# Kernel optimization log

Hardware: AMD Instinct MI355X
Metric: run time of the kernel (lower is better)

The kernel has to match this reference:

```python
import jax, jax.numpy as jnp
import numpy as np

N = 100000   # nodes
E = 1600000  # edges (avg degree 16)
IN, H, OUT, P = 100, 256, 256, 128
EPS = 1e-5


def setup_inputs() -> dict:
    key = jax.random.key(0)
    ks = jax.random.split(key, 12)

    def lin(k, o, i):
        return jax.random.normal(k, (o, i), jnp.float32) / np.float32(np.sqrt(i))

    return {
        "x": jax.random.normal(ks[0], (N, IN), jnp.float32),
        "edge_index": jax.random.randint(ks[1], (2, E), 0, N),
        # SAGEConv l (aggregated-neighbor branch, has bias) and r (root branch, no bias)
        "Wl0": lin(ks[2], H, IN), "bl0": jnp.zeros((H,), jnp.float32), "Wr0": lin(ks[3], H, IN),
        "Wl1": lin(ks[4], H, H),  "bl1": jnp.zeros((H,), jnp.float32), "Wr1": lin(ks[5], H, H),
        "Wl2": lin(ks[6], OUT, H), "bl2": jnp.zeros((OUT,), jnp.float32), "Wr2": lin(ks[7], OUT, H),
        # projection head + BatchNorm1d(128)
        "Wp": lin(ks[8], P, OUT), "bp": jnp.zeros((P,), jnp.float32),
        "gamma": jnp.ones((P,), jnp.float32), "beta": jnp.zeros((P,), jnp.float32),
    }


def _sage_conv(x, src, dst, Wl, bl, Wr):
    # PyG SAGEConv default: mean-aggregate source features into destinations,
    # then lin_l(agg) + lin_r(x).
    agg = jax.ops.segment_sum(x[src], dst, num_segments=N)           # [N, d]
    deg = jax.ops.segment_sum(jnp.ones((src.shape[0],), x.dtype), dst, num_segments=N)
    agg = agg / jnp.maximum(deg, 1.0)[:, None]
    return agg @ Wl.T + bl + x @ Wr.T


def reference(x, edge_index, Wl0, bl0, Wr0, Wl1, bl1, Wr1, Wl2, bl2, Wr2, Wp, bp, gamma, beta):
    src, dst = edge_index[0], edge_index[1]
    x = jax.nn.relu(_sage_conv(x, src, dst, Wl0, bl0, Wr0))  # dropout is identity in eval
    x = jax.nn.relu(_sage_conv(x, src, dst, Wl1, bl1, Wr1))
    x = _sage_conv(x, src, dst, Wl2, bl2, Wr2)               # no relu on last layer
    z = x @ Wp.T + bp                                        # projection head -> [N, 128]
    mu = jnp.mean(z, axis=0)
    var = jnp.var(z, axis=0)                                 # biased, as torch BN uses for normalization
    h = gamma * (z - mu) * jax.lax.rsqrt(var + EPS) + beta
    return (x, h)
```

## Files before the change

### kernel.cpp

```cpp
#include <hip/hip_runtime.h>
#include <hip/hip_bf16.h>

#define EPS_BN 1e-5f

using short8  = __attribute__((ext_vector_type(8))) short;
using ushort8 = __attribute__((ext_vector_type(8))) unsigned short;
using f32x4   = __attribute__((ext_vector_type(4))) float;

typedef const __attribute__((address_space(1))) void* gas_ptr;
typedef __attribute__((address_space(3))) void* las_ptr;

__device__ inline float bf2f(unsigned short u) {
    union { unsigned i; float f; } c; c.i = ((unsigned)u) << 16; return c.f;
}
__device__ inline unsigned short f2bf(float f) {
    unsigned x = __float_as_uint(f);
    unsigned r = (x + 0x7FFF + ((x >> 16) & 1)) >> 16;
    return (unsigned short)r;
}

__global__ void zero_i32(int* __restrict__ p, int n) {
    int i = blockIdx.x * blockDim.x + threadIdx.x;
    if (i < n) p[i] = 0;
}
__global__ void zero_f32(float* __restrict__ p, int n) {
    int i = blockIdx.x * blockDim.x + threadIdx.x;
    if (i < n) p[i] = 0.0f;
}

__global__ void zero_rows(unsigned short* __restrict__ xpad,
                          unsigned short* __restrict__ h1,
                          unsigned short* __restrict__ h2, int n) {
    int t = threadIdx.x;
    if (t < 128) xpad[(size_t)n * 128 + t] = 0;
    h1[(size_t)n * 256 + t] = 0;
    h2[(size_t)n * 256 + t] = 0;
}

__global__ void conv_w(const float* __restrict__ w, unsigned short* __restrict__ o,
                       int R, int C, int CP) {
    int t = blockIdx.x * blockDim.x + threadIdx.x;
    if (t >= R * CP) return;
    int r = t / CP, c = t % CP;
    o[t] = (c < C) ? f2bf(w[(size_t)r * C + c]) : (unsigned short)0;
}

__global__ void conv_x_pad(const float* __restrict__ x, unsigned short* __restrict__ xp, int n) {
    int t = blockIdx.x * blockDim.x + threadIdx.x;
    if (t >= n * 32) return;
    int node = t >> 5, g = t & 31;
    int f0 = g * 4;
    ushort4 o;
    const float* xr = x + (size_t)node * 100;
    o.x = (f0 + 0 < 100) ? f2bf(xr[f0 + 0]) : 0;
    o.y = (f0 + 1 < 100) ? f2bf(xr[f0 + 1]) : 0;
    o.z = (f0 + 2 < 100) ? f2bf(xr[f0 + 2]) : 0;
    o.w = (f0 + 3 < 100) ? f2bf(xr[f0 + 3]) : 0;
    *(ushort4*)(xp + (size_t)node * 128 + f0) = o;
}

__global__ void count_k(const int* __restrict__ dst, int* __restrict__ counts, int E) {
    int i = blockIdx.x * blockDim.x + threadIdx.x;
    if (i < E) atomicAdd(&counts[dst[i]], 1);
}

__global__ void scan1(const int* __restrict__ counts, int* __restrict__ rp,
                      int* __restrict__ partials, int n) {
    __shared__ int s[256];
    int t = threadIdx.x;
    int i = blockIdx.x * 256 + t;
    int v = (i < n) ? ((counts[i] + 7) & ~7) : 0;
    s[t] = v;
    __syncthreads();
    for (int off = 1; off < 256; off <<= 1) {
        int u = (t >= off) ? s[t - off] : 0;
        __syncthreads();
        s[t] += u;
        __syncthreads();
    }
    if (i < n) rp[i] = s[t] - v;
    if (t == 255) partials[blockIdx.x] = s[255];
}

__global__ void scan2(int* __restrict__ partials, int nb) {
    __shared__ int s[512];
    int t = threadIdx.x;
    int v = (t < nb) ? partials[t] : 0;
    s[t] = v;
    __syncthreads();
    for (int off = 1; off < 512; off <<= 1) {
        int u = (t >= off) ? s[t - off] : 0;
        __syncthreads();
        s[t] += u;
        __syncthreads();
    }
    if (t < nb) partials[t] = s[t] - v;
}

__global__ void scan3(int* __restrict__ rp, const int* __restrict__ partials, int n) {
    int i = blockIdx.x * blockDim.x + threadIdx.x;
    if (i < n) rp[i] += partials[i >> 8];
}

__global__ void fill_k(const int* __restrict__ src, const int* __restrict__ dst,
                       const int* __restrict__ rp, int* __restrict__ cursor,
                       int* __restrict__ col, int E) {
    int i = blockIdx.x * blockDim.x + threadIdx.x;
    if (i < E) {
        int d = dst[i];
        int pos = atomicAdd(&cursor[d], 1);
        col[rp[d] + pos] = src[i];
    }
}

__global__ void pad_fill(const int* __restrict__ rp, const int* __restrict__ cnt,
                         int* __restrict__ col, int n, int zrow) {
    int node = blockIdx.x * blockDim.x + threadIdx.x;
    if (node >= n) return;
    int d = cnt[node];
    int s = rp[node] + d;
    int e = rp[node] + ((d + 7) & ~7);
    for (int i = s; i < e; ++i) col[i] = zrow;
}

__global__ __launch_bounds__(256) void agg_bf16_256(
    const unsigned short* __restrict__ x, const int* __restrict__ rp,
    const int* __restrict__ cnt, const int* __restrict__ col,
    unsigned short* __restrict__ out, int n) {
    int wave = threadIdx.x >> 6, lane = threadIdx.x & 63;
    int node = blockIdx.x * 4 + wave;
    if (node >= n) return;
    int s = rp[node];
    int deg = cnt[node];
    int nb8 = (deg + 7) >> 3;
    int h = lane >> 5;
    int l32 = lane & 31;
    const size_t coff = (size_t)l32 * 8;

    float a[8] = {0, 0, 0, 0, 0, 0, 0, 0};
    int i = s + h;
    int b = 0;
    for (; b + 2 <= nb8; b += 2, i += 16) {
        int r0 = col[i],     r1 = col[i + 2],  r2 = col[i + 4],  r3 = col[i + 6];
        int r4 = col[i + 8], r5 = col[i + 10], r6 = col[i + 12], r7 = col[i + 14];
        ushort8 v0 = *(const ushort8*)(x + (size_t)r0 * 256 + coff);
        ushort8 v1 = *(const ushort8*)(x + (size_t)r1 * 256 + coff);
        ushort8 v2 = *(const ushort8*)(x + (size_t)r2 * 256 + coff);
        ushort8 v3 = *(const ushort8*)(x + (size_t)r3 * 256 + coff);
        ushort8 v4 = *(const ushort8*)(x + (size_t)r4 * 256 + coff);
        ushort8 v5 = *(const ushort8*)(x + (size_t)r5 * 256 + coff);
        ushort8 v6 = *(const ushort8*)(x + (size_t)r6 * 256 + coff);
        ushort8 v7 = *(const ushort8*)(x + (size_t)r7 * 256 + coff);
#pragma unroll
        for (int j = 0; j < 8; ++j)
            a[j] += ((bf2f(v0[j]) + bf2f(v1[j])) + (bf2f(v2[j]) + bf2f(v3[j]))) +
                    ((bf2f(v4[j]) + bf2f(v5[j])) + (bf2f(v6[j]) + bf2f(v7[j])));
    }
    if (b < nb8) {
        int r0 = col[i], r1 = col[i + 2], r2 = col[i + 4], r3 = col[i + 6];
        ushort8 v0 = *(const ushort8*)(x + (size_t)r0 * 256 + coff);
        ushort8 v1 = *(const ushort8*)(x + (size_t)r1 * 256 + coff);
        ushort8 v2 = *(const ushort8*)(x + (size_t)r2 * 256 + coff);
        ushort8 v3 = *(const ushort8*)(x + (size_t)r3 * 256 + coff);
#pragma unroll
        for (int j = 0; j < 8; ++j)
            a[j] += (bf2f(v0[j]) + bf2f(v1[j])) + (bf2f(v2[j]) + bf2f(v3[j]));
    }
#pragma unroll
    for (int j = 0; j < 8; ++j) a[j] += __shfl_xor(a[j], 32);

    if (h == 0) {
        float sc = 1.0f / fmaxf((float)deg, 1.0f);
        ushort8 o;
#pragma unroll
        for (int j = 0; j < 8; ++j) o[j] = f2bf(a[j] * sc);
        *(ushort8*)(out + (size_t)node * 256 + l32 * 8) = o;
    }
}

__global__ __launch_bounds__(256) void agg_bf16_128(
    const unsigned short* __restrict__ x, const int* __restrict__ rp,
    const int* __restrict__ cnt, const int* __restrict__ col,
    unsigned short* __restrict__ out, int n) {
    int wave = threadIdx.x >> 6, lane = threadIdx.x & 63;
    int node = blockIdx.x * 4 + wave;
    if (node >= n) return;
    int s = rp[node];
    int deg = cnt[node];
    int nb8 = (deg + 7) >> 3;
    int q = lane >> 4;
    int l16 = lane & 15;
    const size_t coff = (size_t)l16 * 8;

    float a[8] = {0, 0, 0, 0, 0, 0, 0, 0};
    int i = s + q;
    int b = 0;
    for (; b + 2 <= nb8; b += 2, i += 16) {
        int r0 = col[i], r1 = col[i + 4], r2 = col[i + 8], r3 = col[i + 12];
        ushort8 v0 = *(const ushort8*)(x + (size_t)r0 * 128 + coff);
        ushort8 v1 = *(const ushort8*)(x + (size_t)r1 * 128 + coff);
        ushort8 v2 = *(const ushort8*)(x + (size_t)r2 * 128 + coff);
        ushort8 v3 = *(const ushort8*)(x + (size_t)r3 * 128 + coff);
#pragma unroll
        for (int j = 0; j < 8; ++j)
            a[j] += (bf2f(v0[j]) + bf2f(v1[j])) + (bf2f(v2[j]) + bf2f(v3[j]));
    }
    if (b < nb8) {
        int r0 = col[i], r1 = col[i + 4];
        ushort8 v0 = *(const ushort8*)(x + (size_t)r0 * 128 + coff);
        ushort8 v1 = *(const ushort8*)(x + (size_t)r1 * 128 + coff);
#pragma unroll
        for (int j = 0; j < 8; ++j) a[j] += bf2f(v0[j]) + bf2f(v1[j]);
    }
#pragma unroll
    for (int j = 0; j < 8; ++j) {
        a[j] += __shfl_xor(a[j], 16);
        a[j] += __shfl_xor(a[j], 32);
    }

    if (lane < 16) {
        float sc = 1.0f / fmaxf((float)deg, 1.0f);
        ushort8 o;
#pragma unroll
        for (int j = 0; j < 8; ++j) o[j] = f2bf(a[j] * sc);
        *(ushort8*)(out + (size_t)node * 128 + l16 * 8) = o;
    }
}

template <int KTOT, int DOUT, bool HAS_AGG, bool RELU, bool STF32, bool STBF16>
__global__ __launch_bounds__(512) void sage_mfma(
    const unsigned short* __restrict__ xp, const unsigned short* __restrict__ ap,
    const unsigned short* __restrict__ Wr, const unsigned short* __restrict__ Wl,
    const float* __restrict__ bias,
    float* __restrict__ outf, unsigned short* __restrict__ outb, int n) {
    constexpr int CT = DOUT / 16;
    constexpr int NSRC = HAS_AGG ? 2 : 1;
    constexpr int FR = DOUT * 4;
    constexpr int CHUNKS = NSRC * CT;
    constexpr int CPW = CHUNKS / 8;
    constexpr int KS = KTOT / 32;
    constexpr int BUFSZ = NSRC * FR * 8;
    __shared__ __align__(16) unsigned short lds[2 * BUFSZ];

    const int t = threadIdx.x;
    const int wave = t >> 6, lane = t & 63;
    const int node0 = blockIdx.x * 128 + wave * 16;
    const bool active = node0 < n;
    const int lcol = lane & 15, lq = lane >> 4;

    auto stage = [&](int ks, int buf) {
        unsigned short* base = lds + buf * BUFSZ;
#pragma unroll
        for (int i = 0; i < CPW; ++i) {
            int chunk = wave * CPW + i;
            int srcSel = chunk / CT, ct = chunk % CT;
            const unsigned short* W = (srcSel == 0) ? Wr : Wl;
            const unsigned short* g = W + (size_t)(ct * 16 + lcol) * KTOT + ks * 32 + lq * 8;
            unsigned short* l = base + chunk * 512;
            __builtin_amdgcn_global_load_lds((gas_ptr)g, (las_ptr)l, 16, 0, 0);
        }
    };

    f32x4 acc[CT];
#pragma unroll
    for (int c = 0; c < CT; ++c) {
        float b = bias[c * 16 + lcol];
        acc[c][0] = b; acc[c][1] = b; acc[c][2] = b; acc[c][3] = b;
    }

    const unsigned short* aRow  = xp + (size_t)(node0 + lcol) * KTOT + lq * 8;
    const unsigned short* aRow2 = HAS_AGG ? (ap + (size_t)(node0 + lcol) * KTOT + lq * 8) : xp;

    stage(0, 0);
    __syncthreads();

    for (int ks = 0; ks < KS; ++ks) {
        if (ks + 1 < KS) stage(ks + 1, (ks + 1) & 1);
        if (active) {
            short8 a = *(const short8*)(aRow + ks * 32);
            const short8* bf = (const short8*)(lds + (ks & 1) * BUFSZ);
#pragma unroll
            for (int c = 0; c < CT; ++c)
                acc[c] = __builtin_amdgcn_mfma_f32_16x16x32_bf16(a, bf[c * 64 + lane], acc[c], 0, 0, 0);
            if (HAS_AGG) {
                short8 a2 = *(const short8*)(aRow2 + ks * 32);
                const short8* bf2 = bf + FR;
#pragma unroll
                for (int c = 0; c < CT; ++c)
                    acc[c] = __builtin_amdgcn_mfma_f32_16x16x32_bf16(a2, bf2[c * 64 + lane], acc[c], 0, 0, 0);
            }
        }
        __syncthreads();
    }
    if (!active) return;

#pragma unroll
    for (int c = 0; c < CT; ++c) {
        f32x4 v = acc[c];
        if (RELU) {
            v[0] = fmaxf(v[0], 0.0f); v[1] = fmaxf(v[1], 0.0f);
            v[2] = fmaxf(v[2], 0.0f); v[3] = fmaxf(v[3], 0.0f);
        }
#pragma unroll
        for (int j = 0; j < 4; ++j) {
            size_t row = (size_t)node0 + lq * 4 + j;
            int colI = c * 16 + lcol;
            if (STF32) outf[row * DOUT + colI] = v[j];
            if (STBF16) outb[row * DOUT + colI] = f2bf(v[j]);
        }
    }
}

__global__ void bn_partial(const float* __restrict__ z, float* __restrict__ sums, int n) {
    int f = threadIdx.x & 127;
    int half = threadIdx.x >> 7;
    float s = 0.0f, s2 = 0.0f;
    for (int row = blockIdx.x * 2 + half; row < n; row += gridDim.x * 2) {
        float v = z[(size_t)row * 128 + f];
        s += v; s2 += v * v;
    }
    __shared__ float ls[256], ls2[256];
    ls[threadIdx.x] = s; ls2[threadIdx.x] = s2;
    __syncthreads();
    if (half == 0) {
        atomicAdd(&sums[f], s + ls[128 + f]);
        atomicAdd(&sums[128 + f], s2 + ls2[128 + f]);
    }
}

__global__ void bn_finalize(const float* __restrict__ sums, const float* __restrict__ gamma,
                            const float* __restrict__ beta, float* __restrict__ params, int n) {
    int f = threadIdx.x;
    float mu = sums[f] / (float)n;
    float var = sums[128 + f] / (float)n - mu * mu;
    float inv = rsqrtf(var + EPS_BN);
    float sc = gamma[f] * inv;
    params[f] = sc;
    params[128 + f] = beta[f] - mu * sc;
}

__global__ void bn_apply(float* __restrict__ z, const float* __restrict__ params, int total4) {
    int i = blockIdx.x * blockDim.x + threadIdx.x;
    for (; i < total4; i += gridDim.x * blockDim.x) {
        float4 v = ((float4*)z)[i];
        int f0 = (i & 31) * 4;
        v.x = v.x * params[f0 + 0] + params[128 + f0 + 0];
        v.y = v.y * params[f0 + 1] + params[128 + f0 + 1];
        v.z = v.z * params[f0 + 2] + params[128 + f0 + 2];
        v.w = v.w * params[f0 + 3] + params[128 + f0 + 3];
        ((float4*)z)[i] = v;
    }
}

extern "C" void kernel_launch(void* const* d_in, const int* in_sizes, int n_in,
                              void* d_out, int out_size, void* d_ws, size_t ws_size,
                              hipStream_t stream) {
    const float* x_in  = (const float*)d_in[0];
    const int*   ei    = (const int*)d_in[1];
    const float* Wl0   = (const float*)d_in[2];
    const float* bl0   = (const float*)d_in[3];
    const float* Wr0   = (const float*)d_in[4];
    const float* Wl1   = (const float*)d_in[5];
    const float* bl1   = (const float*)d_in[6];
    const float* Wr1   = (const float*)d_in[7];
    const float* Wl2   = (const float*)d_in[8];
    const float* bl2   = (const float*)d_in[9];
    const float* Wr2   = (const float*)d_in[10];
    const float* Wp    = (const float*)d_in[11];
    const float* bp    = (const float*)d_in[12];
    const float* gamma = (const float*)d_in[13];
    const float* beta  = (const float*)d_in[14];

    const int IN = 100, INP = 128, H = 256, OUT = 256, P = 128;
    const int n = in_sizes[0] / IN;
    const int E = in_sizes[1] / 2;
    const int* src = ei;
    const int* dst = ei + E;

    size_t off = 0;
    auto alloc = [&](size_t bytes) -> char* {
        char* p = (char*)d_ws + off;
        off += (bytes + 255) & ~(size_t)255;
        return p;
    };
    int*   counts   = (int*)alloc((size_t)n * 4);
    int*   cursor   = (int*)alloc((size_t)n * 4);
    int*   rp       = (int*)alloc((size_t)(n + 1) * 4);
    int*   partials = (int*)alloc(512 * 4);
    int*   col      = (int*)alloc(((size_t)E + 8 * (size_t)n) * 4);
    unsigned short* Wl0b = (unsigned short*)alloc((size_t)H * INP * 2);
    unsigned short* Wr0b = (unsigned short*)alloc((size_t)H * INP * 2);
    unsigned short* Wl1b = (unsigned short*)alloc((size_t)H * H * 2);
    unsigned short* Wr1b = (unsigned short*)alloc((size_t)H * H * 2);
    unsigned short* Wl2b = (unsigned short*)alloc((size_t)OUT * H * 2);
    unsigned short* Wr2b = (unsigned short*)alloc((size_t)OUT * H * 2);
    unsigned short* Wpb  = (unsigned short*)alloc((size_t)P * OUT * 2);
    float* bnsums   = (float*)alloc(256 * 4);
    float* bnparams = (float*)alloc(256 * 4);
    unsigned short* xpad   = (unsigned short*)alloc((size_t)(n + 1) * INP * 2);
    unsigned short* aggpad = (unsigned short*)alloc((size_t)n * INP * 2);
    unsigned short* h1b    = (unsigned short*)alloc((size_t)(n + 1) * H * 2);
    unsigned short* agg1   = (unsigned short*)alloc((size_t)n * H * 2);
    unsigned short* h2b    = (unsigned short*)alloc((size_t)(n + 1) * H * 2);
    (void)alloc((size_t)256 * 512);

    unsigned short* agg2 = h1b;
    unsigned short* xb2  = xpad;

    float* out_x = (float*)d_out;
    float* z     = out_x + (size_t)n * OUT;

    const int nb = (n + 255) / 256;

    zero_i32<<<nb, 256, 0, stream>>>(counts, n);
    zero_i32<<<nb, 256, 0, stream>>>(cursor, n);
    zero_f32<<<1, 256, 0, stream>>>(bnsums, 256);
    count_k<<<(E + 255) / 256, 256, 0, stream>>>(dst, counts, E);
    scan1<<<nb, 256, 0, stream>>>(counts, rp, partials, n);
    scan2<<<1, 512, 0, stream>>>(partials, nb);
    scan3<<<nb, 256, 0, stream>>>(rp, partials, n);
    fill_k<<<(E + 255) / 256, 256, 0, stream>>>(src, dst, rp, cursor, col, E);
    pad_fill<<<nb, 256, 0, stream>>>(rp, counts, col, n, n);

    conv_x_pad<<<(n * 32 + 255) / 256, 256, 0, stream>>>(x_in, xpad, n);
    zero_rows<<<1, 256, 0, stream>>>(xpad, h1b, h2b, n);
    conv_w<<<(H * INP + 255) / 256, 256, 0, stream>>>(Wl0, Wl0b, H, IN, INP);
    conv_w<<<(H * INP + 255) / 256, 256, 0, stream>>>(Wr0, Wr0b, H, IN, INP);
    conv_w<<<(H * H + 255) / 256, 256, 0, stream>>>(Wl1, Wl1b, H, H, H);
    conv_w<<<(H * H + 255) / 256, 256, 0, stream>>>(Wr1, Wr1b, H, H, H);
    conv_w<<<(OUT * H + 255) / 256, 256, 0, stream>>>(Wl2, Wl2b, OUT, H, H);
    conv_w<<<(OUT * H + 255) / 256, 256, 0, stream>>>(Wr2, Wr2b, OUT, H, H);
    conv_w<<<(P * OUT + 255) / 256, 256, 0, stream>>>(Wp, Wpb, P, OUT, OUT);

    const int gemm_grid = (n + 127) / 128;

    agg_bf16_128<<<(n + 3) / 4, 256, 0, stream>>>(xpad, rp, counts, col, aggpad, n);
    sage_mfma<128, 256, true, true, false, true><<<gemm_grid, 512, 0, stream>>>(
        xpad, aggpad, Wr0b, Wl0b, bl0, nullptr, h1b, n);

    agg_bf16_256<<<(n + 3) / 4, 256, 0, stream>>>(h1b, rp, counts, col, agg1, n);
    sage_mfma<256, 256, true, true, false, true><<<gemm_grid, 512, 0, stream>>>(
        h1b, agg1, Wr1b, Wl1b, bl1, nullptr, h2b, n);

    agg_bf16_256<<<(n + 3) / 4, 256, 0, stream>>>(h2b, rp, counts, col, agg2, n);
    sage_mfma<256, 256, true, false, true, true><<<gemm_grid, 512, 0, stream>>>(
        h2b, agg2, Wr2b, Wl2b, bl2, out_x, xb2, n);

    sage_mfma<256, 128, false, false, true, false><<<gemm_grid, 512, 0, stream>>>(
        xb2, nullptr, Wpb, nullptr, bp, z, nullptr, n);

    bn_partial<<<256, 256, 0, stream>>>(z, bnsums, n);
    bn_finalize<<<1, 128, 0, stream>>>(bnsums, gamma, beta, bnparams, n);
    bn_apply<<<2048, 256, 0, stream>>>(z, bnparams, n * (P / 4));
}
```

Baseline: 746.6 us.

## Retile SAGE MFMA kernel to 2x4 wave grid with register-prefetched A operands

New measurement: 873.0 us. 16.9% more time.

```diff
diff --git a/kernel.cpp b/kernel.cpp
--- a/kernel.cpp
+++ b/kernel.cpp
@@ -234,19 +234,19 @@
     const float* __restrict__ bias,
     float* __restrict__ outf, unsigned short* __restrict__ outb, int n) {
     constexpr int CT = DOUT / 16;
+    constexpr int CTW = DOUT / 64;
     constexpr int NSRC = HAS_AGG ? 2 : 1;
-    constexpr int FR = DOUT * 4;
     constexpr int CHUNKS = NSRC * CT;
     constexpr int CPW = CHUNKS / 8;
     constexpr int KS = KTOT / 32;
-    constexpr int BUFSZ = NSRC * FR * 8;
+    constexpr int BUFSZ = CHUNKS * 512;
     __shared__ __align__(16) unsigned short lds[2 * BUFSZ];
 
     const int t = threadIdx.x;
     const int wave = t >> 6, lane = t & 63;
-    const int node0 = blockIdx.x * 128 + wave * 16;
-    const bool active = node0 < n;
+    const int wm = wave >> 2, wn = wave & 3;
     const int lcol = lane & 15, lq = lane >> 4;
+    const int node0 = blockIdx.x * 128 + wm * 64;
 
     auto stage = [&](int ks, int buf) {
         unsigned short* base = lds + buf * BUFSZ;
@@ -261,52 +261,89 @@
         }
     };
 
-    f32x4 acc[CT];
-#pragma unroll
-    for (int c = 0; c < CT; ++c) {
-        float b = bias[c * 16 + lcol];
-        acc[c][0] = b; acc[c][1] = b; acc[c][2] = b; acc[c][3] = b;
-    }
-
-    const unsigned short* aRow  = xp + (size_t)(node0 + lcol) * KTOT + lq * 8;
-    const unsigned short* aRow2 = HAS_AGG ? (ap + (size_t)(node0 + lcol) * KTOT + lq * 8) : xp;
+    const unsigned short* aPx[4];
+    const unsigned short* aPa[4];
+#pragma unroll
+    for (int mt = 0; mt < 4; ++mt) {
+        aPx[mt] = xp + (size_t)(node0 + mt * 16 + lcol) * KTOT + lq * 8;
+        if (HAS_AGG) aPa[mt] = ap + (size_t)(node0 + mt * 16 + lcol) * KTOT + lq * 8;
+    }
+    auto LOADA = [&](int ks, short8 (&ax)[4], short8 (&aa)[4]) {
+#pragma unroll
+        for (int mt = 0; mt < 4; ++mt) {
+            ax[mt] = *(const short8*)(aPx[mt] + ks * 32);
+            if (HAS_AGG) aa[mt] = *(const short8*)(aPa[mt] + ks * 32);
+        }
+    };
+
+    f32x4 acc[4][CTW];
+#pragma unroll
+    for (int ct = 0; ct < CTW; ++ct) {
+        float b = bias[wn * CTW * 16 + ct * 16 + lcol];
+#pragma unroll
+        for (int mt = 0; mt < 4; ++mt) {
+            acc[mt][ct][0] = b; acc[mt][ct][1] = b; acc[mt][ct][2] = b; acc[mt][ct][3] = b;
+        }
+    }
+
+    auto COMPUTE = [&](int buf, short8 (&ax)[4], short8 (&aa)[4]) {
+        const unsigned short* base = lds + buf * BUFSZ;
+        short8 br[CTW], bl[CTW];
+#pragma unroll
+        for (int c = 0; c < CTW; ++c) {
+            br[c] = *(const short8*)(base + (wn * CTW + c) * 512 + lane * 8);
+            if (HAS_AGG) bl[c] = *(const short8*)(base + (CT + wn * CTW + c) * 512 + lane * 8);
+        }
+#pragma unroll
+        for (int mt = 0; mt < 4; ++mt)
+#pragma unroll
+            for (int c = 0; c < CTW; ++c) {
+                acc[mt][c] = __builtin_amdgcn_mfma_f32_16x16x32_bf16(
+                    ax[mt], br[c], acc[mt][c], 0, 0, 0);
+                if (HAS_AGG)
+                    acc[mt][c] = __builtin_amdgcn_mfma_f32_16x16x32_bf16(
+                        aa[mt], bl[c], acc[mt][c], 0, 0, 0);
+            }
+    };
+
+    short8 axE[4], aaE[4], axO[4], aaO[4];
 
     stage(0, 0);
+    LOADA(0, axE, aaE);
     __syncthreads();
 
-    for (int ks = 0; ks < KS; ++ks) {
-        if (ks + 1 < KS) stage(ks + 1, (ks + 1) & 1);
-        if (active) {
-            short8 a = *(const short8*)(aRow + ks * 32);
-            const short8* bf = (const short8*)(lds + (ks & 1) * BUFSZ);
-#pragma unroll
-            for (int c = 0; c < CT; ++c)
-                acc[c] = __builtin_amdgcn_mfma_f32_16x16x32_bf16(a, bf[c * 64 + lane], acc[c], 0, 0, 0);
-            if (HAS_AGG) {
-                short8 a2 = *(const short8*)(aRow2 + ks * 32);
-                const short8* bf2 = bf + FR;
-#pragma unroll
-                for (int c = 0; c < CT; ++c)
-                    acc[c] = __builtin_amdgcn_mfma_f32_16x16x32_bf16(a2, bf2[c * 64 + lane], acc[c], 0, 0, 0);
+#pragma unroll
+    for (int ks = 0; ks < KS; ks += 2) {
+        if (ks + 1 < KS) { stage(ks + 1, 1); LOADA(ks + 1, axO, aaO); }
+        COMPUTE(0, axE, aaE);
+        __syncthreads();
+        if (ks + 2 < KS) { stage(ks + 2, 0); LOADA(ks + 2, axE, aaE); }
+        if (ks + 1 < KS) {
+            COMPUTE(1, axO, aaO);
+            __syncthreads();
+        }
+    }
+
+#pragma unroll
+    for (int mt = 0; mt < 4; ++mt) {
+        int row0 = node0 + mt * 16 + lq * 4;
+        if (row0 >= n) continue;
+#pragma unroll
+        for (int ct = 0; ct < CTW; ++ct) {
+            f32x4 v = acc[mt][ct];
+            if (RELU) {
+                v[0] = fmaxf(v[0], 0.0f); v[1] = fmaxf(v[1], 0.0f);
+                v[2] = fmaxf(v[2], 0.0f); v[3] = fmaxf(v[3], 0.0f);
             }
-        }
-        __syncthreads();
-    }
-    if (!active) return;
-
-#pragma unroll
-    for (int c = 0; c < CT; ++c) {
-        f32x4 v = acc[c];
-        if (RELU) {
-            v[0] = fmaxf(v[0], 0.0f); v[1] = fmaxf(v[1], 0.0f);
-            v[2] = fmaxf(v[2], 0.0f); v[3] = fmaxf(v[3], 0.0f);
-        }
-#pragma unroll
-        for (int j = 0; j < 4; ++j) {
-            size_t row = (size_t)node0 + lq * 4 + j;
-            int colI = c * 16 + lcol;
-            if (STF32) outf[row * DOUT + colI] = v[j];
-            if (STBF16) outb[row * DOUT + colI] = f2bf(v[j]);
+            int colI = wn * CTW * 16 + ct * 16 + lcol;
+#pragma unroll
+            for (int j = 0; j < 4; ++j) {
+                int row = row0 + j;
+                if (row < n) {
+                    if (STF32) outf[(size_t)row * DOUT + colI] = v[j];
+                    if (STBF16) outb[(size_t)row * DOUT + colI] = f2bf(v[j]);
+                }
+            }
         }
     }
 }
```

## Split GEMM output columns across a second grid dimension and read fp32 projection input

Applied to the files above, without the earlier changes.

Result: slower. 775.7 us (+3.9%).

```diff
diff --git a/kernel.cpp b/kernel.cpp
--- a/kernel.cpp
+++ b/kernel.cpp
@@ -227,15 +227,16 @@
     }
 }
 
-template <int KTOT, int DOUT, bool HAS_AGG, bool RELU, bool STF32, bool STBF16>
+template <int KTOT, int DOUT, int BCOLS, bool HAS_AGG, bool A_F32,
+          bool RELU, bool STF32, bool STBF16>
 __global__ __launch_bounds__(512) void sage_mfma(
-    const unsigned short* __restrict__ xp, const unsigned short* __restrict__ ap,
+    const void* __restrict__ xpv, const unsigned short* __restrict__ ap,
     const unsigned short* __restrict__ Wr, const unsigned short* __restrict__ Wl,
     const float* __restrict__ bias,
     float* __restrict__ outf, unsigned short* __restrict__ outb, int n) {
-    constexpr int CT = DOUT / 16;
+    constexpr int CT = BCOLS / 16;
     constexpr int NSRC = HAS_AGG ? 2 : 1;
-    constexpr int FR = DOUT * 4;
+    constexpr int FR = CT * 64;
     constexpr int CHUNKS = NSRC * CT;
     constexpr int CPW = CHUNKS / 8;
     constexpr int KS = KTOT / 32;
@@ -245,6 +246,7 @@
     const int t = threadIdx.x;
     const int wave = t >> 6, lane = t & 63;
     const int node0 = blockIdx.x * 128 + wave * 16;
+    const int col_base = blockIdx.y * BCOLS;
     const bool active = node0 < n;
     const int lcol = lane & 15, lq = lane >> 4;
 
@@ -255,7 +257,8 @@
             int chunk = wave * CPW + i;
             int srcSel = chunk / CT, ct = chunk % CT;
             const unsigned short* W = (srcSel == 0) ? Wr : Wl;
-            const unsigned short* g = W + (size_t)(ct * 16 + lcol) * KTOT + ks * 32 + lq * 8;
+            const unsigned short* g =
+                W + (size_t)(col_base + ct * 16 + lcol) * KTOT + ks * 32 + lq * 8;
             unsigned short* l = base + chunk * 512;
             __builtin_amdgcn_global_load_lds((gas_ptr)g, (las_ptr)l, 16, 0, 0);
         }
@@ -264,12 +267,16 @@
     f32x4 acc[CT];
 #pragma unroll
     for (int c = 0; c < CT; ++c) {
-        float b = bias[c * 16 + lcol];
+        float b = bias[col_base + c * 16 + lcol];
         acc[c][0] = b; acc[c][1] = b; acc[c][2] = b; acc[c][3] = b;
     }
 
-    const unsigned short* aRow  = xp + (size_t)(node0 + lcol) * KTOT + lq * 8;
-    const unsigned short* aRow2 = HAS_AGG ? (ap + (size_t)(node0 + lcol) * KTOT + lq * 8) : xp;
+    const unsigned short* aRow = nullptr;
+    const float* aRowF = nullptr;
+    if constexpr (A_F32) aRowF = (const float*)xpv + (size_t)(node0 + lcol) * KTOT + lq * 8;
+    else                 aRow  = (const unsigned short*)xpv + (size_t)(node0 + lcol) * KTOT + lq * 8;
+    const unsigned short* aRow2 =
+        HAS_AGG ? (ap + (size_t)(node0 + lcol) * KTOT + lq * 8) : nullptr;
 
     stage(0, 0);
     __syncthreads();
@@ -277,7 +284,17 @@
     for (int ks = 0; ks < KS; ++ks) {
         if (ks + 1 < KS) stage(ks + 1, (ks + 1) & 1);
         if (active) {
-            short8 a = *(const short8*)(aRow + ks * 32);
+            short8 a;
+            if constexpr (A_F32) {
+                float4 f0 = *(const float4*)(aRowF + ks * 32);
+                float4 f1 = *(const float4*)(aRowF + ks * 32 + 4);
+                a[0] = (short)f2bf(f0.x); a[1] = (short)f2bf(f0.y);
+                a[2] = (short)f2bf(f0.z); a[3] = (short)f2bf(f0.w);
+                a[4] = (short)f2bf(f1.x); a[5] = (short)f2bf(f1.y);
+                a[6] = (short)f2bf(f1.z); a[7] = (short)f2bf(f1.w);
+            } else {
+                a = *(const short8*)(aRow + ks * 32);
+            }
             const short8* bf = (const short8*)(lds + (ks & 1) * BUFSZ);
 #pragma unroll
             for (int c = 0; c < CT; ++c)
@@ -304,7 +321,7 @@
 #pragma unroll
         for (int j = 0; j < 4; ++j) {
             size_t row = (size_t)node0 + lq * 4 + j;
-            int colI = c * 16 + lcol;
+            int colI = col_base + c * 16 + lcol;
             if (STF32) outf[row * DOUT + colI] = v[j];
             if (STBF16) outb[row * DOUT + colI] = f2bf(v[j]);
         }
@@ -405,7 +422,6 @@
     (void)alloc((size_t)256 * 512);
 
     unsigned short* agg2 = h1b;
-    unsigned short* xb2  = xpad;
 
     float* out_x = (float*)d_out;
     float* z     = out_x + (size_t)n * OUT;
@@ -432,22 +448,26 @@
     conv_w<<<(OUT * H + 255) / 256, 256, 0, stream>>>(Wr2, Wr2b, OUT, H, H);
     conv_w<<<(P * OUT + 255) / 256, 256, 0, stream>>>(Wp, Wpb, P, OUT, OUT);
 
-    const int gemm_grid = (n + 127) / 128;
+    const int gx = (n + 127) / 128;
 
     agg_bf16_128<<<(n + 3) / 4, 256, 0, stream>>>(xpad, rp, counts, col, aggpad, n);
-    sage_mfma<128, 256, true, true, false, true><<<gemm_grid, 512, 0, stream>>>(
+    sage_mfma<128, 256, 128, true, false, true, false, true>
+        <<<dim3(gx, 2), 512, 0, stream>>>(
         xpad, aggpad, Wr0b, Wl0b, bl0, nullptr, h1b, n);
 
     agg_bf16_256<<<(n + 3) / 4, 256, 0, stream>>>(h1b, rp, counts, col, agg1, n);
-    sage_mfma<256, 256, true, true, false, true><<<gemm_grid, 512, 0, stream>>>(
+    sage_mfma<256, 256, 128, true, false, true, false, true>
+        <<<dim3(gx, 2), 512, 0, stream>>>(
         h1b, agg1, Wr1b, Wl1b, bl1, nullptr, h2b, n);
 
     agg_bf16_256<<<(n + 3) / 4, 256, 0, stream>>>(h2b, rp, counts, col, agg2, n);
-    sage_mfma<256, 256, true, false, true, true><<<gemm_grid, 512, 0, stream>>>(
-        h2b, agg2, Wr2b, Wl2b, bl2, out_x, xb2, n);
-
-    sage_mfma<256, 128, false, false, true, false><<<gemm_grid, 512, 0, stream>>>(
-        xb2, nullptr, Wpb, nullptr, bp, z, nullptr, n);
+    sage_mfma<256, 256, 128, true, false, false, true, false>
+        <<<dim3(gx, 2), 512, 0, stream>>>(
+        h2b, agg2, Wr2b, Wl2b, bl2, out_x, nullptr, n);
+
+    sage_mfma<256, 128, 128, false, true, false, true, false>
+        <<<dim3(gx, 1), 512, 0, stream>>>(
+        out_x, nullptr, Wpb, nullptr, bp, z, nullptr, n);
 
     bn_partial<<<256, 256, 0, stream>>>(z, bnsums, n);
     bn_finalize<<<1, 128, 0, stream>>>(bnsums, gamma, beta, bnparams, n);
```

## Switch SAGE GEMMs to 32x32x16 MFMA with 2D wave tiling

Applied to the files above, without the earlier changes.

New measurement: 768.5 us. 2.9% more time.

```diff
diff --git a/kernel.cpp b/kernel.cpp
--- a/kernel.cpp
+++ b/kernel.cpp
@@ -5,7 +5,7 @@
 
 using short8  = __attribute__((ext_vector_type(8))) short;
 using ushort8 = __attribute__((ext_vector_type(8))) unsigned short;
-using f32x4   = __attribute__((ext_vector_type(4))) float;
+using f32x16  = __attribute__((ext_vector_type(16))) float;
 
 typedef const __attribute__((address_space(1))) void* gas_ptr;
 typedef __attribute__((address_space(3))) void* las_ptr;
@@ -227,49 +227,55 @@
     }
 }
 
-template <int KTOT, int DOUT, bool HAS_AGG, bool RELU, bool STF32, bool STBF16>
+template <int KTOT, int DOUT, int WAVES_M, bool HAS_AGG, bool RELU, bool STF32, bool STBF16>
 __global__ __launch_bounds__(512) void sage_mfma(
     const unsigned short* __restrict__ xp, const unsigned short* __restrict__ ap,
     const unsigned short* __restrict__ Wr, const unsigned short* __restrict__ Wl,
     const float* __restrict__ bias,
     float* __restrict__ outf, unsigned short* __restrict__ outb, int n) {
-    constexpr int CT = DOUT / 16;
+    constexpr int WAVES_N = 8 / WAVES_M;
+    constexpr int NCT = DOUT / 32;
+    constexpr int CTW = NCT / WAVES_N;
     constexpr int NSRC = HAS_AGG ? 2 : 1;
-    constexpr int FR = DOUT * 4;
-    constexpr int CHUNKS = NSRC * CT;
+    constexpr int CHUNKS = NSRC * NCT * 2;
     constexpr int CPW = CHUNKS / 8;
     constexpr int KS = KTOT / 32;
-    constexpr int BUFSZ = NSRC * FR * 8;
+    constexpr int BUFSZ = CHUNKS * 512;
     __shared__ __align__(16) unsigned short lds[2 * BUFSZ];
 
     const int t = threadIdx.x;
     const int wave = t >> 6, lane = t & 63;
-    const int node0 = blockIdx.x * 128 + wave * 16;
+    const int wm = wave / WAVES_N, wn = wave % WAVES_N;
+    const int l32 = lane & 31, lh = lane >> 5;
+    const int node0 = blockIdx.x * (WAVES_M * 32) + wm * 32;
     const bool active = node0 < n;
-    const int lcol = lane & 15, lq = lane >> 4;
 
     auto stage = [&](int ks, int buf) {
         unsigned short* base = lds + buf * BUFSZ;
 #pragma unroll
         for (int i = 0; i < CPW; ++i) {
             int chunk = wave * CPW + i;
-            int srcSel = chunk / CT, ct = chunk % CT;
-            const unsigned short* W = (srcSel == 0) ? Wr : Wl;
-            const unsigned short* g = W + (size_t)(ct * 16 + lcol) * KTOT + ks * 32 + lq * 8;
-            unsigned short* l = base + chunk * 512;
-            __builtin_amdgcn_global_load_lds((gas_ptr)g, (las_ptr)l, 16, 0, 0);
+            int kk = chunk & 1;
+            int ct = (chunk >> 1) % NCT;
+            int s  = (chunk >> 1) / NCT;
+            const unsigned short* W = (s == 0) ? Wr : Wl;
+            const unsigned short* g =
+                W + (size_t)(ct * 32 + l32) * KTOT + ks * 32 + kk * 16 + lh * 8;
+            __builtin_amdgcn_global_load_lds((gas_ptr)g, (las_ptr)(base + chunk * 512),
+                                             16, 0, 0);
         }
     };
 
-    f32x4 acc[CT];
-#pragma unroll
-    for (int c = 0; c < CT; ++c) {
-        float b = bias[c * 16 + lcol];
-        acc[c][0] = b; acc[c][1] = b; acc[c][2] = b; acc[c][3] = b;
-    }
-
-    const unsigned short* aRow  = xp + (size_t)(node0 + lcol) * KTOT + lq * 8;
-    const unsigned short* aRow2 = HAS_AGG ? (ap + (size_t)(node0 + lcol) * KTOT + lq * 8) : xp;
+    f32x16 acc[CTW];
+#pragma unroll
+    for (int c = 0; c < CTW; ++c) {
+        float b = bias[(wn * CTW + c) * 32 + l32];
+#pragma unroll
+        for (int r = 0; r < 16; ++r) acc[c][r] = b;
+    }
+
+    const unsigned short* aRow  = xp + (size_t)(node0 + l32) * KTOT + lh * 8;
+    const unsigned short* aRow2 = HAS_AGG ? (ap + (size_t)(node0 + l32) * KTOT + lh * 8) : xp;
 
     stage(0, 0);
     __syncthreads();
@@ -277,17 +283,25 @@
     for (int ks = 0; ks < KS; ++ks) {
         if (ks + 1 < KS) stage(ks + 1, (ks + 1) & 1);
         if (active) {
-            short8 a = *(const short8*)(aRow + ks * 32);
-            const short8* bf = (const short8*)(lds + (ks & 1) * BUFSZ);
-#pragma unroll
-            for (int c = 0; c < CT; ++c)
-                acc[c] = __builtin_amdgcn_mfma_f32_16x16x32_bf16(a, bf[c * 64 + lane], acc[c], 0, 0, 0);
-            if (HAS_AGG) {
-                short8 a2 = *(const short8*)(aRow2 + ks * 32);
-                const short8* bf2 = bf + FR;
-#pragma unroll
-                for (int c = 0; c < CT; ++c)
-                    acc[c] = __builtin_amdgcn_mfma_f32_16x16x32_bf16(a2, bf2[c * 64 + lane], acc[c], 0, 0, 0);
+            const unsigned short* base = lds + (ks & 1) * BUFSZ;
+#pragma unroll
+            for (int kk = 0; kk < 2; ++kk) {
+                short8 a0 = *(const short8*)(aRow + ks * 32 + kk * 16);
+#pragma unroll
+                for (int c = 0; c < CTW; ++c) {
+                    int chunk = (wn * CTW + c) * 2 + kk;
+                    short8 bfr = *(const short8*)(base + chunk * 512 + lane * 8);
+                    acc[c] = __builtin_amdgcn_mfma_f32_32x32x16_bf16(a0, bfr, acc[c], 0, 0, 0);
+                }
+                if constexpr (HAS_AGG) {
+                    short8 a1 = *(const short8*)(aRow2 + ks * 32 + kk * 16);
+#pragma unroll
+                    for (int c = 0; c < CTW; ++c) {
+                        int chunk = (NCT + wn * CTW + c) * 2 + kk;
+                        short8 bfl = *(const short8*)(base + chunk * 512 + lane * 8);
+                        acc[c] = __builtin_amdgcn_mfma_f32_32x32x16_bf16(a1, bfl, acc[c], 0, 0, 0);
+                    }
+                }
             }
         }
         __syncthreads();
@@ -295,18 +309,15 @@
     if (!active) return;
 
 #pragma unroll
-    for (int c = 0; c < CT; ++c) {
-        f32x4 v = acc[c];
-        if (RELU) {
-            v[0] = fmaxf(v[0], 0.0f); v[1] = fmaxf(v[1], 0.0f);
-            v[2] = fmaxf(v[2], 0.0f); v[3] = fmaxf(v[3], 0.0f);
-        }
-#pragma unroll
-        for (int j = 0; j < 4; ++j) {
-            size_t row = (size_t)node0 + lq * 4 + j;
-            int colI = c * 16 + lcol;
-            if (STF32) outf[row * DOUT + colI] = v[j];
-            if (STBF16) outb[row * DOUT + colI] = f2bf(v[j]);
+    for (int c = 0; c < CTW; ++c) {
+        int colI = (wn * CTW + c) * 32 + l32;
+#pragma unroll
+        for (int r = 0; r < 16; ++r) {
+            float v = acc[c][r];
+            if (RELU) v = fmaxf(v, 0.0f);
+            size_t row = (size_t)node0 + (r & 3) + 8 * (r >> 2) + 4 * lh;
+            if (STF32) outf[row * DOUT + colI] = v;
+            if (STBF16) outb[row * DOUT + colI] = f2bf(v);
         }
     }
 }
@@ -435,18 +446,18 @@
     const int gemm_grid = (n + 127) / 128;
 
     agg_bf16_128<<<(n + 3) / 4, 256, 0, stream>>>(xpad, rp, counts, col, aggpad, n);
-    sage_mfma<128, 256, true, true, false, true><<<gemm_grid, 512, 0, stream>>>(
+    sage_mfma<128, 256, 4, true, true, false, true><<<gemm_grid, 512, 0, stream>>>(
         xpad, aggpad, Wr0b, Wl0b, bl0, nullptr, h1b, n);
 
     agg_bf16_256<<<(n + 3) / 4, 256, 0, stream>>>(h1b, rp, counts, col, agg1, n);
-    sage_mfma<256, 256, true, true, false, true><<<gemm_grid, 512, 0, stream>>>(
+    sage_mfma<256, 256, 4, true, true, false, true><<<gemm_grid, 512, 0, stream>>>(
         h1b, agg1, Wr1b, Wl1b, bl1, nullptr, h2b, n);
 
     agg_bf16_256<<<(n + 3) / 4, 256, 0, stream>>>(h2b, rp, counts, col, agg2, n);
-    sage_mfma<256, 256, true, false, true, true><<<gemm_grid, 512, 0, stream>>>(
+    sage_mfma<256, 256, 4, true, false, true, true><<<gemm_grid, 512, 0, stream>>>(
         h2b, agg2, Wr2b, Wl2b, bl2, out_x, xb2, n);
 
-    sage_mfma<256, 128, false, false, true, false><<<gemm_grid, 512, 0, stream>>>(
+    sage_mfma<256, 128, 8, false, false, true, false><<<(n + 255) / 256, 512, 0, stream>>>(
         xb2, nullptr, Wpb, nullptr, bp, z, nullptr, n);
 
     bn_partial<<<256, 256, 0, stream>>>(z, bnsums, n);
```
